# Kernel tuning notes

Hardware: AMD Instinct MI355X
Metric: run time of the kernel (lower is better)

Reference implementation:

```python
import jax, jax.numpy as jnp
import numpy as np

B = 2048
GIN = 128      # gating input features
GH = 128       # gating hidden units
E = 8          # experts
XIN = 512      # expert input features
U = 512        # expert layer units
OUT = 512      # expert output features


def setup_inputs() -> dict:
    key = jax.random.key(0)
    ks = jax.random.split(key, 16)
    rn = lambda k, shape: (jax.random.normal(k, shape) * 0.05).astype(jnp.float32)
    return {
        "gating_input": jax.random.normal(ks[0], (B, GIN), dtype=jnp.float32),
        "expert_input": jax.random.normal(ks[1], (B, XIN), dtype=jnp.float32),
        # gating MLP params (Dense stores kernel as (in, out))
        "Wg0": rn(ks[2], (GIN, GH)), "bg0": rn(ks[3], (GH,)),
        "Wg1": rn(ks[4], (GH, GH)), "bg1": rn(ks[5], (GH,)),
        "Wgo": rn(ks[6], (GH, E)),  "bgo": rn(ks[7], (E,)),
        # expert weight pools: alpha (E, units, in), beta (E, units)
        "alpha0": rn(ks[8], (E, U, XIN)), "beta0": rn(ks[9], (E, U)),
        "alpha1": rn(ks[10], (E, U, U)),  "beta1": rn(ks[11], (E, U)),
        "alpha2": rn(ks[12], (E, OUT, U)), "beta2": rn(ks[13], (E, OUT)),
    }


def dense_expert(x, g, alpha, beta):
    # Mathematically: (sum_e g[b,e] * alpha[e]) @ x[b] + sum_e g[b,e]*beta[e]
    # Contract input with each expert first (avoids the (B,U,I) blended-weight tensor).
    per_expert = jnp.einsum("bi,eui->beu", x, alpha)   # (B, E, U)
    w = jnp.einsum("be,beu->bu", g, per_expert)         # (B, U)
    b = jnp.einsum("be,eu->bu", g, beta)                # (B, U)
    return w + b


def reference(gating_input, expert_input, Wg0, bg0, Wg1, bg1, Wgo, bgo,
              alpha0, beta0, alpha1, beta1, alpha2, beta2):
    # Gating network: Dense+ELU x2 (dropout is identity at inference), Dense+softmax
    h = jax.nn.elu(gating_input @ Wg0 + bg0)
    h = jax.nn.elu(h @ Wg1 + bg1)
    g = jax.nn.softmax(h @ Wgo + bgo, axis=-1)          # (B, E)

    # Expert network: DenseExpert + ELU x2, final DenseExpert
    x = jax.nn.elu(dense_expert(expert_input, g, alpha0, beta0))
    x = jax.nn.elu(dense_expert(x, g, alpha1, beta1))
    y = dense_expert(x, g, alpha2, beta2)               # (B, OUT)
    return y
```

## Files before the change

kernel.cpp:

```cpp
#include <hip/hip_runtime.h>
#include <math.h>

#define BATCH 2048
#define GIN 128
#define GH 128
#define NE 8
#define XIN 512
#define UU 512

typedef __attribute__((ext_vector_type(8))) short short8;
typedef __attribute__((ext_vector_type(4))) float f32x4;

#define AS1 __attribute__((address_space(1)))
#define AS3 __attribute__((address_space(3)))

__device__ inline unsigned short f2bf(float f) {
    unsigned u = __float_as_uint(f);
    u += 0x7fffu + ((u >> 16) & 1u);
    return (unsigned short)(u >> 16);
}

__device__ inline float elu1(float x) { return x > 0.f ? x : (expf(x) - 1.f); }

__global__ __launch_bounds__(256) void pre_kernel(
    const float* __restrict__ gin, const float* __restrict__ W0, const float* __restrict__ b0,
    const float* __restrict__ W1, const float* __restrict__ b1,
    const float* __restrict__ Wo, const float* __restrict__ bo,
    float* __restrict__ g,
    const float* __restrict__ a0, const float* __restrict__ a1, const float* __restrict__ a2,
    const float* __restrict__ xv, unsigned short* __restrict__ dst)
{
    __shared__ float xs[4][128];
    __shared__ float hs[4][128];
    __shared__ float ps[2][4][128];
    __shared__ float lp[8][4][8];
    __shared__ float ls[4][8];

    const int t = threadIdx.x;

    if (blockIdx.x >= 512) {
        const long long vi = ((long long)(blockIdx.x - 512) * 256 + t) * 4;
        const int sel = (int)(vi >> 21);
        const float* src = (sel == 0) ? a0 : (sel == 1) ? a1 : (sel == 2) ? a2 : xv;
        float4 v = *(const float4*)(src + (vi & ((1 << 21) - 1)));
        union { unsigned short us[4]; uint2 u2; } p;
        p.us[0] = f2bf(v.x); p.us[1] = f2bf(v.y); p.us[2] = f2bf(v.z); p.us[3] = f2bf(v.w);
        *(uint2*)(dst + vi) = p.u2;
        return;
    }

    const int c = t & 127;
    const int h = t >> 7;
    const int row0 = blockIdx.x * 4;

    ((float*)xs)[t]       = gin[row0 * GIN + t];
    ((float*)xs)[t + 256] = gin[row0 * GIN + t + 256];
    __syncthreads();

    {
        float acc0 = 0.f, acc1 = 0.f, acc2 = 0.f, acc3 = 0.f;
        const float* Wc = W0 + c;
        #pragma unroll 8
        for (int i = h * 64; i < h * 64 + 64; ++i) {
            float w = Wc[i * GH];
            acc0 += xs[0][i] * w; acc1 += xs[1][i] * w;
            acc2 += xs[2][i] * w; acc3 += xs[3][i] * w;
        }
        ps[h][0][c] = acc0; ps[h][1][c] = acc1; ps[h][2][c] = acc2; ps[h][3][c] = acc3;
    }
    __syncthreads();
    {
        int o = t, r = o >> 7, cc = o & 127;
        hs[r][cc] = elu1(ps[0][r][cc] + ps[1][r][cc] + b0[cc]);
        o = t + 256; r = o >> 7; cc = o & 127;
        hs[r][cc] = elu1(ps[0][r][cc] + ps[1][r][cc] + b0[cc]);
    }
    __syncthreads();

    {
        float acc0 = 0.f, acc1 = 0.f, acc2 = 0.f, acc3 = 0.f;
        const float* Wc = W1 + c;
        #pragma unroll 8
        for (int i = h * 64; i < h * 64 + 64; ++i) {
            float w = Wc[i * GH];
            acc0 += hs[0][i] * w; acc1 += hs[1][i] * w;
            acc2 += hs[2][i] * w; acc3 += hs[3][i] * w;
        }
        ps[h][0][c] = acc0; ps[h][1][c] = acc1; ps[h][2][c] = acc2; ps[h][3][c] = acc3;
    }
    __syncthreads();
    {
        int o = t, r = o >> 7, cc = o & 127;
        xs[r][cc] = elu1(ps[0][r][cc] + ps[1][r][cc] + b1[cc]);
        o = t + 256; r = o >> 7; cc = o & 127;
        xs[r][cc] = elu1(ps[0][r][cc] + ps[1][r][cc] + b1[cc]);
    }
    __syncthreads();

    {
        const int e = t & 7, r = (t >> 3) & 3, q = t >> 5;
        float s = 0.f;
        #pragma unroll
        for (int i = q * 16; i < q * 16 + 16; ++i) s += xs[r][i] * Wo[i * NE + e];
        lp[q][r][e] = s;
    }
    __syncthreads();
    if (t < 32) {
        const int r = t >> 3, e = t & 7;
        float s = bo[e];
        #pragma unroll
        for (int q = 0; q < 8; ++q) s += lp[q][r][e];
        ls[r][e] = s;
    }
    __syncthreads();
    if (t < 4) {
        float mx = ls[t][0];
        #pragma unroll
        for (int e = 1; e < 8; ++e) mx = fmaxf(mx, ls[t][e]);
        float s = 0.f, ex[8];
        #pragma unroll
        for (int e = 0; e < 8; ++e) { ex[e] = expf(ls[t][e] - mx); s += ex[e]; }
        float inv = 1.f / s;
        #pragma unroll
        for (int e = 0; e < 8; ++e) g[(row0 + t) * NE + e] = ex[e] * inv;
    }
}

__global__ __launch_bounds__(256) void moe_layer_kernel(
    const unsigned short* __restrict__ A,
    const unsigned short* __restrict__ Bw,
    const float* __restrict__ g,
    const float* __restrict__ beta,
    unsigned short* __restrict__ Xnext,
    float* __restrict__ out, int last)
{
    constexpr int K = XIN;
    __shared__ unsigned short As[2][64 * 32];
    __shared__ float red[4][64][32];
    __shared__ float gs[64][8];
    __shared__ float bt[8][32];

    const int t = threadIdx.x;
    const int bid = blockIdx.x;
    const int n0 = (bid & 15) * 32;
    const int m0 = (bid >> 4) * 64;
    const int wave = t >> 6, lane = t & 63;
    const int e0 = 2 * wave;

    ((float2*)gs)[t] = ((const float2*)(g + (size_t)m0 * NE))[t];
    bt[t >> 5][t & 31] = beta[(t >> 5) * UU + n0 + (t & 31)];

    f32x4 acc[2][4][2] = {};

    const int slot = t & 3;
    const int arow = t >> 2;
    const int acol = ((slot ^ ((arow >> 1) & 3)) * 8);
    const unsigned short* a_src = A + (size_t)(m0 + arow) * K + acol;

    const int fr = lane & 15;
    const int kq = (lane >> 4) * 8;
    const unsigned short* b_ptr[2][2];
    #pragma unroll
    for (int ep = 0; ep < 2; ++ep)
        #pragma unroll
        for (int j = 0; j < 2; ++j)
            b_ptr[ep][j] = Bw + ((size_t)(e0 + ep) * UU + n0 + j * 16 + fr) * K + kq;

#define STAGE_A(bi, ki)                                                      \
    __builtin_amdgcn_global_load_lds(                                        \
        (const AS1 void*)(a_src + (ki)),                                     \
        (AS3 void*)(&As[bi][t * 8]), 16, 0, 0)

#define LOADB(dst, ki)                                                       \
    do {                                                                     \
        dst[0] = *(const short8*)(b_ptr[0][0] + (ki));                       \
        dst[1] = *(const short8*)(b_ptr[0][1] + (ki));                       \
        dst[2] = *(const short8*)(b_ptr[1][0] + (ki));                       \
        dst[3] = *(const short8*)(b_ptr[1][1] + (ki));                       \
    } while (0)

#define COMPUTE(bi, bf)                                                      \
    do {                                                                     \
        const int fkb_ = (lane >> 4) * 16;                                   \
        const char* Ab_ = (const char*)(&As[bi][0]);                         \
        short8 af_[4];                                                       \
        _Pragma("unroll")                                                    \
        for (int i = 0; i < 4; ++i) {                                        \
            const int row_ = fr + i * 16;                                    \
            af_[i] = *(const short8*)(Ab_ +                                  \
                     ((row_ * 64 + fkb_) ^ (((row_ >> 1) & 3) << 4)));       \
        }                                                                    \
        _Pragma("unroll")                                                    \
        for (int ep = 0; ep < 2; ++ep)                                       \
            _Pragma("unroll")                                                \
            for (int i = 0; i < 4; ++i)                                      \
                _Pragma("unroll")                                            \
                for (int j = 0; j < 2; ++j)                                  \
                    acc[ep][i][j] = __builtin_amdgcn_mfma_f32_16x16x32_bf16( \
                        af_[i], bf[ep * 2 + j], acc[ep][i][j], 0, 0, 0);     \
    } while (0)

    short8 bb0[4], bb1[4];

    STAGE_A(0, 0);
    LOADB(bb0, 0);
    __syncthreads();

    #pragma unroll
    for (int s = 0; s < 16; ++s) {
        if (s < 15) {
            STAGE_A((s + 1) & 1, (s + 1) * 32);
            if (s & 1) LOADB(bb0, (s + 1) * 32);
            else       LOADB(bb1, (s + 1) * 32);
        }
        if (s & 1) COMPUTE(1, bb1);
        else       COMPUTE(0, bb0);
        __syncthreads();
    }

    const int cl = lane & 15, rq = lane >> 4;
    #pragma unroll
    for (int i = 0; i < 4; ++i)
        #pragma unroll
        for (int j = 0; j < 2; ++j)
            #pragma unroll
            for (int r = 0; r < 4; ++r) {
                const int rl = i * 16 + rq * 4 + r;
                const int co = j * 16 + cl;
                const float v =
                    gs[rl][e0]     * (acc[0][i][j][r] + bt[e0][co]) +
                    gs[rl][e0 + 1] * (acc[1][i][j][r] + bt[e0 + 1][co]);
                red[wave][rl][co] = v;
            }
    __syncthreads();

    {
        const int rl = t >> 2;
        const int c0 = (t & 3) * 8;
        float v[8];
        #pragma unroll
        for (int u = 0; u < 8; ++u)
            v[u] = red[0][rl][c0 + u] + red[1][rl][c0 + u] +
                   red[2][rl][c0 + u] + red[3][rl][c0 + u];
        if (last) {
            float4 o0 = {v[0], v[1], v[2], v[3]};
            float4 o1 = {v[4], v[5], v[6], v[7]};
            float* op = out + (size_t)(m0 + rl) * UU + n0 + c0;
            *(float4*)op = o0;
            *(float4*)(op + 4) = o1;
        } else {
            union { unsigned short us[8]; short8 s8; } p;
            #pragma unroll
            for (int u = 0; u < 8; ++u) p.us[u] = f2bf(elu1(v[u]));
            *(short8*)(Xnext + (size_t)(m0 + rl) * UU + n0 + c0) = p.s8;
        }
    }
#undef STAGE_A
#undef LOADB
#undef COMPUTE
}

extern "C" void kernel_launch(void* const* d_in, const int* in_sizes, int n_in,
                              void* d_out, int out_size, void* d_ws, size_t ws_size,
                              hipStream_t stream)
{
    (void)in_sizes; (void)n_in; (void)out_size; (void)ws_size;
    const float* gin = (const float*)d_in[0];
    const float* xin = (const float*)d_in[1];
    const float* W0  = (const float*)d_in[2];
    const float* b0  = (const float*)d_in[3];
    const float* W1  = (const float*)d_in[4];
    const float* b1  = (const float*)d_in[5];
    const float* Wo  = (const float*)d_in[6];
    const float* bo  = (const float*)d_in[7];
    const float* alpha[3] = {(const float*)d_in[8],  (const float*)d_in[10], (const float*)d_in[12]};
    const float* beta[3]  = {(const float*)d_in[9],  (const float*)d_in[11], (const float*)d_in[13]};
    float* out = (float*)d_out;

    char* ws = (char*)d_ws;
    float* g = (float*)ws;
    size_t off = 65536;
    unsigned short* ab = (unsigned short*)(ws + off);
    off += (size_t)3 * (1 << 21) * 2;
    unsigned short* Xb0 = (unsigned short*)(ws + off);
    off += (size_t)BATCH * XIN * 2;
    unsigned short* Xb1 = (unsigned short*)(ws + off);
    off += (size_t)BATCH * XIN * 2;

    pre_kernel<<<512 + 7168, 256, 0, stream>>>(
        gin, W0, b0, W1, b1, Wo, bo, g,
        alpha[0], alpha[1], alpha[2], xin, ab);

    unsigned short* Xsrc = Xb0;
    unsigned short* Xdst = Xb1;
    for (int l = 0; l < 3; ++l) {
        moe_layer_kernel<<<512, 256, 0, stream>>>(
            Xsrc, ab + (size_t)l * (1 << 21), g, beta[l], Xdst, out, l == 2 ? 1 : 0);
        unsigned short* tmp = Xsrc; Xsrc = Xdst; Xdst = tmp;
    }
}
```

Baseline: 162.6 us.

## Load A fragments directly to registers, drop LDS staging and loop barriers

The A-tile is no longer staged through shared memory with global_load_lds. Each wave now loads its own A fragments straight from global memory into registers, alongside the B fragments, using a two-deep register double buffer with manual vmcnt waits. This removes the per-iteration __syncthreads and the LDS reads. In exchange, all four waves redundantly fetch the same A rows from global/L2 (four times the A traffic), and register pressure goes up.

```diff
diff --git a/kernel.cpp b/kernel.cpp
--- a/kernel.cpp
+++ b/kernel.cpp
@@ -10,9 +10,6 @@
 
 typedef __attribute__((ext_vector_type(8))) short short8;
 typedef __attribute__((ext_vector_type(4))) float f32x4;
-
-#define AS1 __attribute__((address_space(1)))
-#define AS3 __attribute__((address_space(3)))
 
 __device__ inline unsigned short f2bf(float f) {
     unsigned u = __float_as_uint(f);
@@ -135,7 +132,6 @@
     float* __restrict__ out, int last)
 {
     constexpr int K = XIN;
-    __shared__ unsigned short As[2][64 * 32];
     __shared__ float red[4][64][32];
     __shared__ float gs[64][8];
     __shared__ float bt[8][32];
@@ -146,50 +142,40 @@
     const int m0 = (bid >> 4) * 64;
     const int wave = t >> 6, lane = t & 63;
     const int e0 = 2 * wave;
+    const int fr = lane & 15;
+    const int kq = (lane >> 4) * 8;
 
     ((float2*)gs)[t] = ((const float2*)(g + (size_t)m0 * NE))[t];
     bt[t >> 5][t & 31] = beta[(t >> 5) * UU + n0 + (t & 31)];
+    __syncthreads();
 
     f32x4 acc[2][4][2] = {};
 
-    const int slot = t & 3;
-    const int arow = t >> 2;
-    const int acol = ((slot ^ ((arow >> 1) & 3)) * 8);
-    const unsigned short* a_src = A + (size_t)(m0 + arow) * K + acol;
-
-    const int fr = lane & 15;
-    const int kq = (lane >> 4) * 8;
-    const unsigned short* b_ptr[2][2];
+    const unsigned short* a_ptr[4];
+    #pragma unroll
+    for (int i = 0; i < 4; ++i)
+        a_ptr[i] = A + (size_t)(m0 + fr + i * 16) * K + kq;
+    const unsigned short* b_ptr[4];
     #pragma unroll
     for (int ep = 0; ep < 2; ++ep)
         #pragma unroll
         for (int j = 0; j < 2; ++j)
-            b_ptr[ep][j] = Bw + ((size_t)(e0 + ep) * UU + n0 + j * 16 + fr) * K + kq;
-
-#define STAGE_A(bi, ki)                                                      \
-    __builtin_amdgcn_global_load_lds(                                        \
-        (const AS1 void*)(a_src + (ki)),                                     \
-        (AS3 void*)(&As[bi][t * 8]), 16, 0, 0)
-
-#define LOADB(dst, ki)                                                       \
+            b_ptr[ep * 2 + j] = Bw + ((size_t)(e0 + ep) * UU + n0 + j * 16 + fr) * K + kq;
+
+#define LOADT(aa, bb, ki)                                                    \
     do {                                                                     \
-        dst[0] = *(const short8*)(b_ptr[0][0] + (ki));                       \
-        dst[1] = *(const short8*)(b_ptr[0][1] + (ki));                       \
-        dst[2] = *(const short8*)(b_ptr[1][0] + (ki));                       \
-        dst[3] = *(const short8*)(b_ptr[1][1] + (ki));                       \
+        aa[0] = *(const short8*)(a_ptr[0] + (ki));                           \
+        aa[1] = *(const short8*)(a_ptr[1] + (ki));                           \
+        aa[2] = *(const short8*)(a_ptr[2] + (ki));                           \
+        aa[3] = *(const short8*)(a_ptr[3] + (ki));                           \
+        bb[0] = *(const short8*)(b_ptr[0] + (ki));                           \
+        bb[1] = *(const short8*)(b_ptr[1] + (ki));                           \
+        bb[2] = *(const short8*)(b_ptr[2] + (ki));                           \
+        bb[3] = *(const short8*)(b_ptr[3] + (ki));                           \
     } while (0)
 
-#define COMPUTE(bi, bf)                                                      \
+#define COMPUTE(aa, bb)                                                      \
     do {                                                                     \
-        const int fkb_ = (lane >> 4) * 16;                                   \
-        const char* Ab_ = (const char*)(&As[bi][0]);                         \
-        short8 af_[4];                                                       \
-        _Pragma("unroll")                                                    \
-        for (int i = 0; i < 4; ++i) {                                        \
-            const int row_ = fr + i * 16;                                    \
-            af_[i] = *(const short8*)(Ab_ +                                  \
-                     ((row_ * 64 + fkb_) ^ (((row_ >> 1) & 3) << 4)));       \
-        }                                                                    \
         _Pragma("unroll")                                                    \
         for (int ep = 0; ep < 2; ++ep)                                       \
             _Pragma("unroll")                                                \
@@ -197,25 +183,25 @@
                 _Pragma("unroll")                                            \
                 for (int j = 0; j < 2; ++j)                                  \
                     acc[ep][i][j] = __builtin_amdgcn_mfma_f32_16x16x32_bf16( \
-                        af_[i], bf[ep * 2 + j], acc[ep][i][j], 0, 0, 0);     \
+                        aa[i], bb[ep * 2 + j], acc[ep][i][j], 0, 0, 0);      \
     } while (0)
 
-    short8 bb0[4], bb1[4];
-
-    STAGE_A(0, 0);
-    LOADB(bb0, 0);
-    __syncthreads();
+    short8 aa0[4], aa1[4], bb0[4], bb1[4];
+
+    LOADT(aa0, bb0, 0);
+    LOADT(aa1, bb1, 32);
 
     #pragma unroll
     for (int s = 0; s < 16; ++s) {
-        if (s < 15) {
-            STAGE_A((s + 1) & 1, (s + 1) * 32);
-            if (s & 1) LOADB(bb0, (s + 1) * 32);
-            else       LOADB(bb1, (s + 1) * 32);
-        }
-        if (s & 1) COMPUTE(1, bb1);
-        else       COMPUTE(0, bb0);
-        __syncthreads();
+        if (s < 15) asm volatile("s_waitcnt vmcnt(8)" ::: "memory");
+        else        asm volatile("s_waitcnt vmcnt(0)" ::: "memory");
+        if (s & 1) {
+            COMPUTE(aa1, bb1);
+            if (s + 2 < 16) LOADT(aa1, bb1, (s + 2) * 32);
+        } else {
+            COMPUTE(aa0, bb0);
+            if (s + 2 < 16) LOADT(aa0, bb0, (s + 2) * 32);
+        }
     }
 
     const int cl = lane & 15, rq = lane >> 4;
@@ -255,8 +241,7 @@
             *(short8*)(Xnext + (size_t)(m0 + rl) * UU + n0 + c0) = p.s8;
         }
     }
-#undef STAGE_A
-#undef LOADB
+#undef LOADT
 #undef COMPUTE
 }
 
```

Measured after the change: 200.8 us. +23.5%, slower.
